# Kernel optimization log

Measured on AMD Instinct MI355X. Metric: run time of the kernel, lower is better.

Reference implementation:

```python
import jax, jax.numpy as jnp
import numpy as np

NUM_HEADS = 16
HEAD_SIZE = 64
N_EMBD = 1024


def setup_inputs() -> dict:
    key = jax.random.key(0)
    ks = jax.random.split(key, 6)
    B, T, C = 2, 2048, N_EMBD
    scale = 0.02
    return {
        "x": jax.random.normal(ks[0], (B, T, C), dtype=jnp.float32),
        "Wq": jax.random.normal(ks[1], (C, NUM_HEADS * HEAD_SIZE), dtype=jnp.float32) * scale,
        "Wk": jax.random.normal(ks[2], (C, NUM_HEADS * HEAD_SIZE), dtype=jnp.float32) * scale,
        "Wv": jax.random.normal(ks[3], (C, NUM_HEADS * HEAD_SIZE), dtype=jnp.float32) * scale,
        "Wo": jax.random.normal(ks[4], (NUM_HEADS * HEAD_SIZE, C), dtype=jnp.float32) * scale,
        "bo": jnp.zeros((C,), dtype=jnp.float32),
    }


def reference(x, Wq, Wk, Wv, Wo, bo):
    B, T, C = x.shape
    H, D = NUM_HEADS, HEAD_SIZE
    # QKV projections (no bias), reshape to [B, H, T, D]
    q = (x @ Wq).reshape(B, T, H, D).transpose(0, 2, 1, 3)
    k = (x @ Wk).reshape(B, T, H, D).transpose(0, 2, 1, 3)
    v = (x @ Wv).reshape(B, T, H, D).transpose(0, 2, 1, 3)
    # scaled dot-product scores [B, H, T, T]
    scores = jnp.einsum("bhqd,bhkd->bhqk", q, k) / jnp.sqrt(jnp.float32(D))
    causal = jnp.tril(jnp.ones((T, T), dtype=bool))
    scores = jnp.where(causal, scores, -jnp.inf)
    weights = jax.nn.softmax(scores, axis=-1)  # dropout = identity (eval)
    out = jnp.einsum("bhqk,bhkd->bhqd", weights, v)
    out = out.transpose(0, 2, 1, 3).reshape(B, T, H * D)
    return out @ Wo + bo
```

## Files before the change

### kernel.cpp

```cpp
#include <hip/hip_runtime.h>

typedef __attribute__((ext_vector_type(8))) _Float16 f16x8;
typedef __attribute__((ext_vector_type(2))) _Float16 f16x2;
typedef __attribute__((ext_vector_type(2))) __fp16   fp16x2_raw;
typedef __attribute__((ext_vector_type(4))) float    f32x4;

#define NUM_HEADS 16
#define HEAD_D 64
#define EMB 1024
#define SEQ 2048
#define BATCH 2
#define MTOT (BATCH * SEQ)

#define QALPHA 0.18033688011112042f

__device__ __forceinline__ f16x2 cvt_pk_f16(float lo, float hi)
{
    fp16x2_raw r = __builtin_amdgcn_cvt_pkrtz(lo, hi);
    return __builtin_bit_cast(f16x2, r);
}

#if defined(__has_builtin)
#if __has_builtin(__builtin_amdgcn_exp2f)
#define HAVE_EXP2 1
#endif
#endif
__device__ __forceinline__ float fast_exp2(float x)
{
#ifdef HAVE_EXP2
    return __builtin_amdgcn_exp2f(x);
#else
    return __expf(x * 0.6931471805599453f);
#endif
}

#if defined(__has_builtin)
#if __has_builtin(__builtin_amdgcn_global_load_lds)
#define HAVE_GLOAD_LDS 1
#endif
#endif

__device__ __forceinline__ void stage16(const void* g, void* ldsWaveBase, int lane)
{
#ifdef HAVE_GLOAD_LDS
    __builtin_amdgcn_global_load_lds(
        (const __attribute__((address_space(1))) void*)g,
        (__attribute__((address_space(3))) void*)ldsWaveBase, 16, 0, 0);
    (void)lane;
#else
    *(f16x8*)((char*)ldsWaveBase + lane * 16) = *(const f16x8*)g;
#endif
}

__global__ __launch_bounds__(256) void prep_all(
    const float* __restrict__ x,
    const float* __restrict__ Wq, const float* __restrict__ Wk,
    const float* __restrict__ Wv, const float* __restrict__ Wo,
    _Float16* __restrict__ xh, _Float16* __restrict__ Wt,
    _Float16* __restrict__ Wto)
{
    const int z = blockIdx.z;
    if (z == 4) {
        int base = ((blockIdx.y * 32 + blockIdx.x) * 256 + threadIdx.x) * 2;
        #pragma unroll
        for (int t = 0; t < 2; ++t) {
            int i = base + t;
            float4 a = ((const float4*)x)[i * 2];
            float4 b = ((const float4*)x)[i * 2 + 1];
            f16x8 o;
            o[0] = (_Float16)a.x; o[1] = (_Float16)a.y;
            o[2] = (_Float16)a.z; o[3] = (_Float16)a.w;
            o[4] = (_Float16)b.x; o[5] = (_Float16)b.y;
            o[6] = (_Float16)b.z; o[7] = (_Float16)b.w;
            ((f16x8*)xh)[i] = o;
        }
        return;
    }
    const float* W = z == 0 ? Wq : (z == 1 ? Wk : (z == 2 ? Wv : Wo));
    _Float16* D = (z == 3) ? Wto : (Wt + (size_t)z * EMB * EMB);
    __shared__ float tile[32][33];
    const int tx = threadIdx.x & 31, ty = threadIdx.x >> 5;
    const int n0 = blockIdx.x * 32, k0 = blockIdx.y * 32;
    #pragma unroll
    for (int j = 0; j < 4; ++j)
        tile[ty + j * 8][tx] = W[(size_t)(k0 + ty + j * 8) * EMB + n0 + tx];
    __syncthreads();
    #pragma unroll
    for (int j = 0; j < 4; ++j)
        D[(size_t)(n0 + ty + j * 8) * EMB + k0 + tx] =
            (_Float16)tile[tx][ty + j * 8];
}

__global__ __launch_bounds__(256) void transpose_v(
    const _Float16* __restrict__ Vh, _Float16* __restrict__ VhT)
{
    __shared__ _Float16 tile[64][72];
    const int t0 = blockIdx.x << 6, bh = blockIdx.y;
    const size_t hb  = (size_t)bh * SEQ * HEAD_D;
    const size_t hb2 = (size_t)bh * HEAD_D * SEQ;
    const int tid = threadIdx.x;
    #pragma unroll
    for (int i = 0; i < 2; ++i) {
        int c = (i << 8) + tid, row = c >> 3, u = c & 7;
        f16x8 v = *(const f16x8*)&Vh[hb + (size_t)(t0 + row) * HEAD_D + (u << 3)];
        #pragma unroll
        for (int j = 0; j < 8; ++j)
            tile[(u << 3) + j][row] = v[j];
    }
    __syncthreads();
    #pragma unroll
    for (int i = 0; i < 2; ++i) {
        int c = (i << 8) + tid, row = c >> 3, u = c & 7;
        *(f16x8*)&VhT[hb2 + (size_t)row * SEQ + t0 + (u << 3)] =
            *(const f16x8*)&tile[row][u << 3];
    }
}

template <int MODE>
__global__ __launch_bounds__(256) void gemm_mfma(
    const _Float16* __restrict__ A, const _Float16* __restrict__ Bt,
    _Float16* __restrict__ Qh, _Float16* __restrict__ Kh,
    _Float16* __restrict__ Vh,
    float* __restrict__ outf, const float* __restrict__ bias)
{
    __shared__ __align__(16) _Float16 As[128 * 32];
    __shared__ __align__(16) _Float16 Bs[128 * 32];

    const int tid = threadIdx.x;
    const int w = tid >> 6, lane = tid & 63;
    const int l15 = lane & 15, g4 = lane >> 4;
    const int wm = w >> 1, wn = w & 1;
    const int row0 = blockIdx.y * 128, col0 = blockIdx.x * 128;

    f32x4 acc[4][4];
    #pragma unroll
    for (int mt = 0; mt < 4; ++mt)
        #pragma unroll
        for (int nt = 0; nt < 4; ++nt)
            acc[mt][nt] = (f32x4){0.f, 0.f, 0.f, 0.f};

    for (int k0 = 0; k0 < EMB; k0 += 32) {
        __syncthreads();
        #pragma unroll
        for (int i = 0; i < 2; ++i) {
            int c = (i << 8) + tid;
            int row = c >> 2, u = c & 3;
            stage16(&A[(size_t)(row0 + row) * EMB + k0 + (u << 3)],
                    (char*)As + (i << 12) + (w << 10), lane);
            stage16(&Bt[(size_t)(col0 + row) * EMB + k0 + (u << 3)],
                    (char*)Bs + (i << 12) + (w << 10), lane);
        }
        __syncthreads();

        f16x8 af[4], bf[4];
        #pragma unroll
        for (int mt = 0; mt < 4; ++mt)
            af[mt] = *(const f16x8*)((const char*)As +
                     ((wm << 6) + (mt << 4) + l15) * 64 + (g4 << 4));
        #pragma unroll
        for (int nt = 0; nt < 4; ++nt)
            bf[nt] = *(const f16x8*)((const char*)Bs +
                     ((wn << 6) + (nt << 4) + l15) * 64 + (g4 << 4));
        #pragma unroll
        for (int mt = 0; mt < 4; ++mt)
            #pragma unroll
            for (int nt = 0; nt < 4; ++nt)
                acc[mt][nt] = __builtin_amdgcn_mfma_f32_16x16x32_f16(
                    af[mt], bf[nt], acc[mt][nt], 0, 0, 0);
    }

    #pragma unroll
    for (int mt = 0; mt < 4; ++mt) {
        int m = row0 + (wm << 6) + (mt << 4) + (g4 << 2);
        #pragma unroll
        for (int nt = 0; nt < 4; ++nt) {
            int gcol = col0 + (wn << 6) + (nt << 4) + l15;
            if (MODE == 0) {
                int proj = gcol >> 10, pc = gcol & 1023;
                int h = pc >> 6, d = pc & 63;
                _Float16* dst = proj == 0 ? Qh : (proj == 1 ? Kh : Vh);
                float alpha = proj == 0 ? QALPHA : 1.0f;
                int b = m >> 11, t = m & 2047;
                #pragma unroll
                for (int r = 0; r < 4; ++r)
                    dst[(((size_t)(b * NUM_HEADS + h)) * SEQ + t + r) * HEAD_D + d] =
                        (_Float16)(acc[mt][nt][r] * alpha);
            } else {
                float bz = bias[gcol];
                #pragma unroll
                for (int r = 0; r < 4; ++r)
                    outf[(size_t)(m + r) * EMB + gcol] = acc[mt][nt][r] + bz;
            }
        }
    }
}

__device__ __forceinline__ void stage_kv_tile(
    const _Float16* __restrict__ KhB, const _Float16* __restrict__ VtB,
    int kv0, char* __restrict__ KsBuf, char* __restrict__ VtBuf,
    int w, int lane)
{
    #pragma unroll
    for (int i = 0; i < 2; ++i) {
        int c = (i << 8) + (w << 6) + lane;
        int row = c >> 3, u = c & 7;
        int us = u ^ (row & 7);
        stage16(&KhB[(size_t)(kv0 + row) * HEAD_D + (us << 3)],
                KsBuf + (i << 12) + (w << 10), lane);
        stage16(&VtB[(size_t)row * SEQ + kv0 + (us << 3)],
                VtBuf + (i << 12) + (w << 10), lane);
    }
}

__device__ __forceinline__ void attn_tile(
    const char* __restrict__ KsC, const char* __restrict__ VtC,
    char* __restrict__ pwv,
    f16x8 qf0, f16x8 qf1, f32x4 (&acc)[4], float& m, float& l,
    bool diag, int qrel, int l15, int g)
{
    f32x4 st[4];
    #pragma unroll
    for (int nt = 0; nt < 4; ++nt) {
        int kvl = (nt << 4) + l15;
        f16x8 kf0 = *(const f16x8*)&KsC[kvl * 128 + (((g << 4)) ^ ((kvl & 7) << 4))];
        f16x8 kf1 = *(const f16x8*)&KsC[kvl * 128 + ((64 + (g << 4)) ^ ((kvl & 7) << 4))];
        f32x4 z = (f32x4){0.f, 0.f, 0.f, 0.f};
        z = __builtin_amdgcn_mfma_f32_16x16x32_f16(kf0, qf0, z, 0, 0, 0);
        z = __builtin_amdgcn_mfma_f32_16x16x32_f16(kf1, qf1, z, 0, 0, 0);
        st[nt] = z;
    }
    if (diag) {
        #pragma unroll
        for (int nt = 0; nt < 4; ++nt)
            #pragma unroll
            for (int r = 0; r < 4; ++r)
                if ((nt << 4) + (g << 2) + r > qrel) st[nt][r] = -1e30f;
    }

    float mx;
    {
        float a0 = fmaxf(fmaxf(st[0][0], st[0][1]), fmaxf(st[0][2], st[0][3]));
        float a1 = fmaxf(fmaxf(st[1][0], st[1][1]), fmaxf(st[1][2], st[1][3]));
        float a2 = fmaxf(fmaxf(st[2][0], st[2][1]), fmaxf(st[2][2], st[2][3]));
        float a3 = fmaxf(fmaxf(st[3][0], st[3][1]), fmaxf(st[3][2], st[3][3]));
        mx = fmaxf(fmaxf(a0, a1), fmaxf(a2, a3));
    }
    mx = fmaxf(mx, __shfl_xor(mx, 16));
    mx = fmaxf(mx, __shfl_xor(mx, 32));

    if (!__all(mx - m <= 8.0f)) {
        float nm = fmaxf(m, mx);
        float sc = fast_exp2(m - nm);
        m = nm;
        l *= sc;
        #pragma unroll
        for (int r = 0; r < 4; ++r) {
            float scr = __shfl(sc, (g << 2) + r);
            acc[0][r] *= scr; acc[1][r] *= scr;
            acc[2][r] *= scr; acc[3][r] *= scr;
        }
    }

    float ps = 0.f;
    #pragma unroll
    for (int nt = 0; nt < 4; ++nt)
        #pragma unroll
        for (int r = 0; r < 4; ++r) {
            float p = fast_exp2(st[nt][r] - m);
            st[nt][r] = p;
            ps += p;
        }
    ps += __shfl_xor(ps, 16);
    ps += __shfl_xor(ps, 32);
    l += ps;

    #pragma unroll
    for (int nt = 0; nt < 4; ++nt)
        #pragma unroll
        for (int rr = 0; rr < 2; ++rr) {
            int kvb = (nt << 4) + (g << 2) + (rr << 1);
            f16x2 pv = cvt_pk_f16(st[nt][rr * 2], st[nt][rr * 2 + 1]);
            *(f16x2*)&pwv[l15 * 128 + ((kvb << 1) ^ ((l15 & 7) << 4))] = pv;
        }
    f16x8 pa0 = *(const f16x8*)&pwv[l15 * 128 + (((g << 4)) ^ ((l15 & 7) << 4))];
    f16x8 pa1 = *(const f16x8*)&pwv[l15 * 128 + ((64 + (g << 4)) ^ ((l15 & 7) << 4))];

    #pragma unroll
    for (int dn = 0; dn < 4; ++dn) {
        int d = (dn << 4) + l15;
        f16x8 vf0 = *(const f16x8*)&VtC[d * 128 + (((g << 4)) ^ ((d & 7) << 4))];
        f16x8 vf1 = *(const f16x8*)&VtC[d * 128 + ((64 + (g << 4)) ^ ((d & 7) << 4))];
        acc[dn] = __builtin_amdgcn_mfma_f32_16x16x32_f16(pa0, vf0, acc[dn], 0, 0, 0);
        acc[dn] = __builtin_amdgcn_mfma_f32_16x16x32_f16(pa1, vf1, acc[dn], 0, 0, 0);
    }
}

__global__ __launch_bounds__(256) void attn_mfma(
    const _Float16* __restrict__ Qh, const _Float16* __restrict__ Kh,
    const _Float16* __restrict__ VhT, _Float16* __restrict__ O)
{
    __shared__ char lds[48 * 1024];

    const int qtA = blockIdx.x;
    const int qtB = (SEQ / 64 - 1) - qtA;
    const int bh = blockIdx.y;
    const int q0A = qtA << 6, q0B = qtB << 6;
    const int tid = threadIdx.x;
    const int w = tid >> 6, lane = tid & 63;
    const int l15 = lane & 15, g = lane >> 4;

    const _Float16* KhB = Kh  + (size_t)bh * SEQ * HEAD_D;
    const _Float16* VtB = VhT + (size_t)bh * HEAD_D * SEQ;
    const size_t headbase = (size_t)bh * SEQ * HEAD_D;

    const int qrowA = q0A + (w << 4) + l15;
    const int qrowB = q0B + (w << 4) + l15;
    f16x8 qfA0 = *(const f16x8*)&Qh[headbase + (size_t)qrowA * HEAD_D + (g << 3)];
    f16x8 qfA1 = *(const f16x8*)&Qh[headbase + (size_t)qrowA * HEAD_D + 32 + (g << 3)];
    f16x8 qfB0 = *(const f16x8*)&Qh[headbase + (size_t)qrowB * HEAD_D + (g << 3)];
    f16x8 qfB1 = *(const f16x8*)&Qh[headbase + (size_t)qrowB * HEAD_D + 32 + (g << 3)];

    f32x4 accA[4], accB[4];
    #pragma unroll
    for (int dn = 0; dn < 4; ++dn) {
        accA[dn] = (f32x4){0.f, 0.f, 0.f, 0.f};
        accB[dn] = (f32x4){0.f, 0.f, 0.f, 0.f};
    }
    float mA = -1e30f, lA = 0.f, mB = -1e30f, lB = 0.f;

    stage_kv_tile(KhB, VtB, 0, lds, lds + 16384, w, lane);
    __syncthreads();

    char* pwvA = lds + 32768 + (w << 11);
    char* pwvB = lds + 40960 + (w << 11);

    int cur = 0;
    for (int kt = 0; kt <= qtB; ++kt) {
        if (kt < qtB)
            stage_kv_tile(KhB, VtB, (kt + 1) << 6,
                          lds + ((cur ^ 1) << 13),
                          lds + 16384 + ((cur ^ 1) << 13), w, lane);

        const char* KsC = lds + (cur << 13);
        const char* VtC = lds + 16384 + (cur << 13);
        const int qrel = (w << 4) + l15;

        if (kt <= qtA) {
            attn_tile(KsC, VtC, pwvA, qfA0, qfA1, accA, mA, lA,
                      kt == qtA, qrel, l15, g);
            attn_tile(KsC, VtC, pwvB, qfB0, qfB1, accB, mB, lB,
                      false, qrel, l15, g);
        } else {
            attn_tile(KsC, VtC, pwvB, qfB0, qfB1, accB, mB, lB,
                      kt == qtB, qrel, l15, g);
        }

        __syncthreads();
        cur ^= 1;
    }

    const int b = bh >> 4, h = bh & 15;
    const float rlA = 1.f / lA, rlB = 1.f / lB;
    #pragma unroll
    for (int r = 0; r < 4; ++r) {
        float invA = __shfl(rlA, (g << 2) + r);
        float invB = __shfl(rlB, (g << 2) + r);
        int tokA = (b << 11) + q0A + (w << 4) + (g << 2) + r;
        int tokB = (b << 11) + q0B + (w << 4) + (g << 2) + r;
        #pragma unroll
        for (int dn = 0; dn < 4; ++dn) {
            O[(size_t)tokA * EMB + (h << 6) + (dn << 4) + l15] =
                (_Float16)(accA[dn][r] * invA);
            O[(size_t)tokB * EMB + (h << 6) + (dn << 4) + l15] =
                (_Float16)(accB[dn][r] * invB);
        }
    }
}

extern "C" void kernel_launch(void* const* d_in, const int* in_sizes, int n_in,
                              void* d_out, int out_size, void* d_ws, size_t ws_size,
                              hipStream_t stream)
{
    const float* x  = (const float*)d_in[0];
    const float* Wq = (const float*)d_in[1];
    const float* Wk = (const float*)d_in[2];
    const float* Wv = (const float*)d_in[3];
    const float* Wo = (const float*)d_in[4];
    const float* bo = (const float*)d_in[5];
    float* out = (float*)d_out;

    const size_t ME = (size_t)MTOT * EMB;
    const size_t WE = (size_t)EMB * EMB;
    const size_t need = (6 * ME + 4 * WE) * sizeof(_Float16);
    if (ws_size < need) return;

    _Float16* xh  = (_Float16*)d_ws;
    _Float16* Wt  = xh + ME;
    _Float16* Wto = Wt + 3 * WE;
    _Float16* Qh  = Wto + WE;
    _Float16* Kh  = Qh + ME;
    _Float16* Vh  = Kh + ME;
    _Float16* Ow  = Vh + ME;
    _Float16* VhT = Ow + ME;

    prep_all<<<dim3(EMB / 32, EMB / 32, 5), 256, 0, stream>>>(
        x, Wq, Wk, Wv, Wo, xh, Wt, Wto);

    gemm_mfma<0><<<dim3(3 * EMB / 128, MTOT / 128), 256, 0, stream>>>(
        xh, Wt, Qh, Kh, Vh, nullptr, nullptr);

    transpose_v<<<dim3(SEQ / 64, BATCH * NUM_HEADS), 256, 0, stream>>>(Vh, VhT);

    attn_mfma<<<dim3(SEQ / 128, BATCH * NUM_HEADS), 256, 0, stream>>>(Qh, Kh, VhT, Ow);

    gemm_mfma<1><<<dim3(EMB / 128, MTOT / 128), 256, 0, stream>>>(
        Ow, Wto, nullptr, nullptr, nullptr, out, bo);
}
```

Baseline: 125.0 us.

## Fuse V transpose into QKV GEMM epilogue and raise MFMA wave priority

The QKV projection GEMM now writes V directly in transposed [bh, d, t] layout, using 4-element vector stores along the sequence dimension. This removes the separate transpose_v kernel launch, its extra read and write of V, and one workspace buffer. The attention tile also wraps its two MFMA blocks in s_setprio(1)/s_setprio(0) so waves issuing matrix ops get scheduling priority. The V stores become strided by SEQ per d column, which may coalesce worse than the previous row-major stores.

```diff
diff --git a/kernel.cpp b/kernel.cpp
--- a/kernel.cpp
+++ b/kernel.cpp
@@ -1,6 +1,7 @@
 #include <hip/hip_runtime.h>
 
 typedef __attribute__((ext_vector_type(8))) _Float16 f16x8;
+typedef __attribute__((ext_vector_type(4))) _Float16 f16x4;
 typedef __attribute__((ext_vector_type(2))) _Float16 f16x2;
 typedef __attribute__((ext_vector_type(2))) __fp16   fp16x2_raw;
 typedef __attribute__((ext_vector_type(4))) float    f32x4;
@@ -91,36 +92,11 @@
             (_Float16)tile[tx][ty + j * 8];
 }
 
-__global__ __launch_bounds__(256) void transpose_v(
-    const _Float16* __restrict__ Vh, _Float16* __restrict__ VhT)
-{
-    __shared__ _Float16 tile[64][72];
-    const int t0 = blockIdx.x << 6, bh = blockIdx.y;
-    const size_t hb  = (size_t)bh * SEQ * HEAD_D;
-    const size_t hb2 = (size_t)bh * HEAD_D * SEQ;
-    const int tid = threadIdx.x;
-    #pragma unroll
-    for (int i = 0; i < 2; ++i) {
-        int c = (i << 8) + tid, row = c >> 3, u = c & 7;
-        f16x8 v = *(const f16x8*)&Vh[hb + (size_t)(t0 + row) * HEAD_D + (u << 3)];
-        #pragma unroll
-        for (int j = 0; j < 8; ++j)
-            tile[(u << 3) + j][row] = v[j];
-    }
-    __syncthreads();
-    #pragma unroll
-    for (int i = 0; i < 2; ++i) {
-        int c = (i << 8) + tid, row = c >> 3, u = c & 7;
-        *(f16x8*)&VhT[hb2 + (size_t)row * SEQ + t0 + (u << 3)] =
-            *(const f16x8*)&tile[row][u << 3];
-    }
-}
-
 template <int MODE>
 __global__ __launch_bounds__(256) void gemm_mfma(
     const _Float16* __restrict__ A, const _Float16* __restrict__ Bt,
     _Float16* __restrict__ Qh, _Float16* __restrict__ Kh,
-    _Float16* __restrict__ Vh,
+    _Float16* __restrict__ VhT,
     float* __restrict__ outf, const float* __restrict__ bias)
 {
     __shared__ __align__(16) _Float16 As[128 * 32];
@@ -178,13 +154,23 @@
             if (MODE == 0) {
                 int proj = gcol >> 10, pc = gcol & 1023;
                 int h = pc >> 6, d = pc & 63;
-                _Float16* dst = proj == 0 ? Qh : (proj == 1 ? Kh : Vh);
-                float alpha = proj == 0 ? QALPHA : 1.0f;
                 int b = m >> 11, t = m & 2047;
-                #pragma unroll
-                for (int r = 0; r < 4; ++r)
-                    dst[(((size_t)(b * NUM_HEADS + h)) * SEQ + t + r) * HEAD_D + d] =
-                        (_Float16)(acc[mt][nt][r] * alpha);
+                int bh = b * NUM_HEADS + h;
+                if (proj == 2) {
+                    f16x4 v4;
+                    v4[0] = (_Float16)acc[mt][nt][0];
+                    v4[1] = (_Float16)acc[mt][nt][1];
+                    v4[2] = (_Float16)acc[mt][nt][2];
+                    v4[3] = (_Float16)acc[mt][nt][3];
+                    *(f16x4*)&VhT[((size_t)bh * HEAD_D + d) * SEQ + t] = v4;
+                } else {
+                    _Float16* dst = proj == 0 ? Qh : Kh;
+                    float alpha = proj == 0 ? QALPHA : 1.0f;
+                    #pragma unroll
+                    for (int r = 0; r < 4; ++r)
+                        dst[((size_t)bh * SEQ + t + r) * HEAD_D + d] =
+                            (_Float16)(acc[mt][nt][r] * alpha);
+                }
             } else {
                 float bz = bias[gcol];
                 #pragma unroll
@@ -219,6 +205,7 @@
     bool diag, int qrel, int l15, int g)
 {
     f32x4 st[4];
+    __builtin_amdgcn_s_setprio(1);
     #pragma unroll
     for (int nt = 0; nt < 4; ++nt) {
         int kvl = (nt << 4) + l15;
@@ -229,6 +216,7 @@
         z = __builtin_amdgcn_mfma_f32_16x16x32_f16(kf1, qf1, z, 0, 0, 0);
         st[nt] = z;
     }
+    __builtin_amdgcn_s_setprio(0);
     if (diag) {
         #pragma unroll
         for (int nt = 0; nt < 4; ++nt)
@@ -285,6 +273,7 @@
     f16x8 pa0 = *(const f16x8*)&pwv[l15 * 128 + (((g << 4)) ^ ((l15 & 7) << 4))];
     f16x8 pa1 = *(const f16x8*)&pwv[l15 * 128 + ((64 + (g << 4)) ^ ((l15 & 7) << 4))];
 
+    __builtin_amdgcn_s_setprio(1);
     #pragma unroll
     for (int dn = 0; dn < 4; ++dn) {
         int d = (dn << 4) + l15;
@@ -293,6 +282,7 @@
         acc[dn] = __builtin_amdgcn_mfma_f32_16x16x32_f16(pa0, vf0, acc[dn], 0, 0, 0);
         acc[dn] = __builtin_amdgcn_mfma_f32_16x16x32_f16(pa1, vf1, acc[dn], 0, 0, 0);
     }
+    __builtin_amdgcn_s_setprio(0);
 }
 
 __global__ __launch_bounds__(256) void attn_mfma(
@@ -391,7 +381,7 @@
 
     const size_t ME = (size_t)MTOT * EMB;
     const size_t WE = (size_t)EMB * EMB;
-    const size_t need = (6 * ME + 4 * WE) * sizeof(_Float16);
+    const size_t need = (5 * ME + 4 * WE) * sizeof(_Float16);
     if (ws_size < need) return;
 
     _Float16* xh  = (_Float16*)d_ws;
@@ -399,17 +389,14 @@
     _Float16* Wto = Wt + 3 * WE;
     _Float16* Qh  = Wto + WE;
     _Float16* Kh  = Qh + ME;
-    _Float16* Vh  = Kh + ME;
-    _Float16* Ow  = Vh + ME;
-    _Float16* VhT = Ow + ME;
+    _Float16* VhT = Kh + ME;
+    _Float16* Ow  = VhT + ME;
 
     prep_all<<<dim3(EMB / 32, EMB / 32, 5), 256, 0, stream>>>(
         x, Wq, Wk, Wv, Wo, xh, Wt, Wto);
 
     gemm_mfma<0><<<dim3(3 * EMB / 128, MTOT / 128), 256, 0, stream>>>(
-        xh, Wt, Qh, Kh, Vh, nullptr, nullptr);
-
-    transpose_v<<<dim3(SEQ / 64, BATCH * NUM_HEADS), 256, 0, stream>>>(Vh, VhT);
+        xh, Wt, Qh, Kh, VhT, nullptr, nullptr);
 
     attn_mfma<<<dim3(SEQ / 128, BATCH * NUM_HEADS), 256, 0, stream>>>(Qh, Kh, VhT, Ow);
 
```

Measured after the change: 122.6 us. About the same (-1.9%).
